# Kernel tuning notes

Hardware: AMD Instinct MI355X
Metric: run time of the kernel (lower is better)

## Reference

```python
import jax, jax.numpy as jnp
import numpy as np
from jax import lax

B, E, K, CAP, NC, TC = 512, 8, 2, 160, 10, 256
EPS = 1e-5
CHANS = [(32, 3), (64, 32), (128, 64), (256, 128)]

def _conv(x, w, b):
    y = lax.conv_general_dilated(x, w, (1, 1), 'SAME', dimension_numbers=('NCHW', 'OIHW', 'NCHW'))
    return y + b[None, :, None, None]

def _bn(x, g, bt, m, v):
    # eval-mode batchnorm with running stats
    s = g / jnp.sqrt(v + EPS)
    return x * s[None, :, None, None] + (bt - m * s)[None, :, None, None]

def _maxpool2(x):
    return lax.reduce_window(x, -jnp.inf, lax.max, (1, 1, 2, 2), (1, 1, 2, 2), 'VALID')

def _trunk(x, ps):
    for i in range(4):
        w, b, g, bt, rm, rv = ps[i]
        x = jax.nn.relu(_bn(_conv(x, w, b), g, bt, rm, rv))
        if i in (1, 3):
            x = _maxpool2(x)
    return x.mean(axis=(2, 3))  # AdaptiveAvgPool2d(1) + Flatten -> [B, TC]

def _route(conf):
    total_needed = B * K
    per_cycle = (total_needed + 3) // 4

    def item_body(c, idx):
        D, ec, sc, assigned, cyc = c
        b, j = idx // E, idx % E
        ok = (~D[b, j]) & (ec[j] < CAP) & (sc[b] < K) & (cyc < per_cycle) & (assigned < total_needed)
        oki = ok.astype(jnp.int32)
        return (D.at[b, j].set(D[b, j] | ok), ec.at[j].add(oki), sc.at[b].add(oki), assigned + oki, cyc + oki), None

    def cycle_body(carry, _):
        D, ec, sc, assigned, current = carry
        order = jnp.argsort(-current.reshape(-1)).astype(jnp.int32)  # descending sort of B*E scores
        (D, ec, sc, assigned, _), _ = lax.scan(item_body, (D, ec, sc, assigned, jnp.int32(0)), order)
        current = conf * (1.0 - ec.astype(jnp.float32) / CAP)[None, :]
        return (D, ec, sc, assigned, current), None

    init = (jnp.zeros((B, E), bool), jnp.zeros((E,), jnp.int32), jnp.zeros((B,), jnp.int32), jnp.int32(0), conf)
    (D, ec, sc, assigned, cur), _ = lax.scan(cycle_body, init, None, length=4)
    return D

def _forward(x, params, cls_w, cls_b):
    feats = _trunk(x, params)                                     # [B, TC]
    logits = jnp.einsum('bd,ecd->bec', feats, cls_w) + cls_b[None]  # [B, E, NC]
    logp = jax.nn.log_softmax(logits, axis=2)
    conf = (jnp.exp(logp) * logp).sum(axis=2)                     # -entropy  [B, E]
    D = _route(lax.stop_gradient(conf))                           # [B, E] bool
    w = jnp.where(D, conf, 0.0)
    final = jnp.einsum('be,bec->bc', w, logits)
    norm = jnp.maximum(D.sum(axis=1, keepdims=True).astype(jnp.float32), 1.0)
    return final / norm, conf, D

def setup_inputs():
    key = jax.random.key(0)
    ks = jax.random.split(key, 8)
    inp = {'x': jax.random.normal(ks[0], (B, 3, 32, 32), jnp.float32)}
    for i, (co, ci) in enumerate(CHANS):
        inp[f'w{i}'] = jax.random.normal(ks[1 + i], (co, ci, 3, 3), jnp.float32) * (2.0 / (ci * 9)) ** 0.5
        inp[f'b{i}'] = jnp.zeros((co,), jnp.float32)
        inp[f'g{i}'] = jnp.ones((co,), jnp.float32)
        inp[f'bt{i}'] = jnp.zeros((co,), jnp.float32)
        inp[f'rm{i}'] = jnp.zeros((co,), jnp.float32)
        inp[f'rv{i}'] = jnp.ones((co,), jnp.float32)
    inp['cls_w'] = jax.random.normal(ks[5], (E, NC, TC), jnp.float32) / TC ** 0.5
    inp['cls_b'] = jnp.zeros((E, NC), jnp.float32)
    return inp

def reference(x, w0, b0, g0, bt0, rm0, rv0, w1, b1, g1, bt1, rm1, rv1, w2, b2, g2, bt2, rm2, rv2, w3, b3, g3, bt3, rm3, rv3, cls_w, cls_b):
    params = [(w0, b0, g0, bt0, rm0, rv0), (w1, b1, g1, bt1, rm1, rv1), (w2, b2, g2, bt2, rm2, rv2), (w3, b3, g3, bt3, rm3, rv3)]
    return _forward(x, params, cls_w, cls_b)
```

## Files before the change

kernel.cpp:

```cpp
#include <hip/hip_runtime.h>
#include <hip/hip_bf16.h>
#include <cstdint>
#include <cstddef>

#define EPSV 1e-5f
typedef unsigned short u16;
using short8 = __attribute__((ext_vector_type(8))) short;
using f32x4  = __attribute__((ext_vector_type(4))) float;

typedef __attribute__((address_space(1))) void* gp1;
typedef __attribute__((address_space(3))) void* lp3;

__device__ __forceinline__ void gload16(const void* g, void* l) {
    __builtin_amdgcn_global_load_lds((gp1)(void*)g, (lp3)l, 16, 0, 0);
}
__device__ __forceinline__ u16 f2bf(float v) {
    __hip_bfloat16 h = __float2bfloat16(v);
    return *reinterpret_cast<u16*>(&h);
}
__device__ __forceinline__ float bf2f(u16 u) {
    __hip_bfloat16 h; *reinterpret_cast<u16*>(&h) = u;
    return __bfloat162float(h);
}

template<int PH2, int PW2, int C>
__global__ __launch_bounds__(256) void ring_kernel(u16* __restrict__ bh, u16* __restrict__ bl)
{
    constexpr int RN = 2 * PW2 + 2 * (PH2 - 2);
    constexpr int C8 = C / 8;
    int id = blockIdx.x * 256 + (int)threadIdx.x;
    if (id >= 512 * RN * C8) return;
    int c8 = id % C8; int t = id / C8;
    int rp = t % RN;  int im = t / RN;
    int py, px;
    if (rp < PW2)            { py = 0;       px = rp; }
    else if (rp < 2 * PW2)   { py = PH2 - 1; px = rp - PW2; }
    else { int rr = rp - 2 * PW2; py = 1 + (rr >> 1); px = (rr & 1) ? (PW2 - 1) : 0; }
    size_t off = ((size_t)(im * PH2 + py) * PW2 + px) * C + c8 * 8;
    uint4 z = {0u, 0u, 0u, 0u};
    *(uint4*)(bh + off) = z;
    *(uint4*)(bl + off) = z;
}

template<int CIN, int COUT>
__global__ __launch_bounds__(256) void wprep_kernel(
    const float* __restrict__ w, const float* __restrict__ b,
    const float* __restrict__ g, const float* __restrict__ bt,
    const float* __restrict__ rm, const float* __restrict__ rv,
    u16* __restrict__ WH, u16* __restrict__ WL, float* __restrict__ bias)
{
    int id = blockIdx.x * 256 + (int)threadIdx.x;
    if (id >= CIN * COUT) return;
    int co = id / CIN, ci = id % CIN;
    float s = g[co] / sqrtf(rv[co] + EPSV);
    #pragma unroll
    for (int k = 0; k < 9; ++k) {
        float v = w[((size_t)co * CIN + ci) * 9 + k] * s;
        u16 hh = f2bf(v);
        size_t o = ((size_t)k * COUT + co) * CIN + ci;
        WH[o] = hh;
        WL[o] = f2bf(v - bf2f(hh));
    }
    if (ci == 0) bias[co] = (b[co] - rm[co]) * s + bt[co];
}

__global__ __launch_bounds__(256) void conv0_kernel(
    const float* __restrict__ x, const float* __restrict__ w,
    const float* __restrict__ bias, const float* __restrict__ g,
    const float* __restrict__ bt, const float* __restrict__ rm,
    const float* __restrict__ rv, u16* __restrict__ Oh, u16* __restrict__ Ol)
{
    const int blk = blockIdx.x;
    const int img = blk >> 2;
    const int p = ((blk & 3) << 8) | (int)threadIdx.x;
    const int y = p >> 5, xx = p & 31;
    const float* xin = x + (size_t)img * 3 * 1024;
    float xv[3][9];
    #pragma unroll
    for (int ci = 0; ci < 3; ++ci)
      #pragma unroll
      for (int ky = 0; ky < 3; ++ky)
        #pragma unroll
        for (int kx = 0; kx < 3; ++kx) {
            int yy = y + ky - 1, xc = xx + kx - 1;
            bool v = (yy >= 0) && (yy < 32) && (xc >= 0) && (xc < 32);
            xv[ci][ky * 3 + kx] = v ? xin[ci * 1024 + yy * 32 + xc] : 0.0f;
        }
    union { u16 u[32]; uint4 v4[4]; } oh, ol;
    #pragma unroll
    for (int co = 0; co < 32; ++co) {
        float s = g[co] / sqrtf(rv[co] + EPSV);
        float c = (bias[co] - rm[co]) * s + bt[co];
        float acc = 0.f;
        #pragma unroll
        for (int ci = 0; ci < 3; ++ci)
          #pragma unroll
          for (int k = 0; k < 9; ++k)
            acc += w[(co * 3 + ci) * 9 + k] * xv[ci][k];
        float v = acc * s + c;
        v = v > 0.f ? v : 0.f;
        u16 hh = f2bf(v);
        oh.u[co] = hh;
        ol.u[co] = f2bf(v - bf2f(hh));
    }
    size_t po = ((size_t)(img * 34 + y + 1) * 34 + xx + 1) * 32;
    #pragma unroll
    for (int q = 0; q < 4; ++q) {
        ((uint4*)(Oh + po))[q] = oh.v4[q];
        ((uint4*)(Ol + po))[q] = ol.v4[q];
    }
}

template<int CIN, int COUT, int H, int W, int BM, int BN, int MODE>
__global__ __launch_bounds__(256, 2) void convM_kernel(
    const u16* __restrict__ Ah, const u16* __restrict__ Al,
    const u16* __restrict__ Wh, const u16* __restrict__ Wl,
    const float* __restrict__ bias,
    u16* __restrict__ Oh, u16* __restrict__ Ol, float* __restrict__ featsPart)
{
    constexpr int KC = CIN / 32;
    constexpr int ROWS = BM / W;
    constexpr int WM = BM / 64;
    constexpr int PW = W + 2;
    constexpr int AT = (ROWS + 2) * PW;
    constexpr int ACH = AT * 4;
    constexpr int BCH = BN * 4;
    constexpr int LW2 = (W == 32) ? 5 : 4;
    constexpr int MPI = (H * W) / BM;

    __shared__ u16 lA[2][AT * 32];
    __shared__ u16 lB[2][BN * 32];

    const int tid = (int)threadIdx.x;
    const int lane = tid & 63;
    const int wv = tid >> 6;
    const int wm = (WM == 4) ? wv : (wv >> 1);
    const int wn = (WM == 4) ? 0 : (wv & 1);
    const int l15 = lane & 15, quad = lane >> 4;

    const int mblk = (int)blockIdx.x, nblk = (int)blockIdx.y;
    const int img = mblk / MPI;
    const int y0 = (mblk % MPI) * ROWS;
    const size_t imgRow = (size_t)img * (H + 2);

    f32x4 acc[4][4];
    f32x4 zz = {0.f, 0.f, 0.f, 0.f};
    #pragma unroll
    for (int i = 0; i < 4; ++i)
      #pragma unroll
      for (int j = 0; j < 4; ++j) acc[i][j] = zz;

    for (int cb = 0; cb < KC; ++cb) {
        __syncthreads();
        #pragma unroll
        for (int it = 0; it < (ACH + 255) / 256; ++it) {
            int id = it * 256 + tid;
            if (id < ACH) {
                int p = id >> 2, s = id & 3;
                int yy = p / PW, xx = p - yy * PW;
                size_t ge = ((imgRow + y0 + yy) * PW + xx) * CIN + cb * 32 + s * 8;
                u16* ld = (u16*)&lA[0][0] + (size_t)(it * 256 + wv * 64) * 8;
                gload16(Ah + ge, ld);
                gload16(Al + ge, ld + AT * 32);
            }
        }
        for (int sh = 0; sh < 9; ++sh) {
            const int ky = sh / 3, kx = sh - 3 * (sh / 3);
            if (sh) __syncthreads();
            #pragma unroll
            for (int it = 0; it < (BCH + 255) / 256; ++it) {
                int id = it * 256 + tid;
                if (id < BCH) {
                    int n = id >> 2, s = id & 3;
                    size_t ge = ((size_t)sh * COUT + nblk * BN + n) * CIN + cb * 32 + s * 8;
                    u16* ld = (u16*)&lB[0][0] + (size_t)(it * 256 + wv * 64) * 8;
                    gload16(Wh + ge, ld);
                    gload16(Wl + ge, ld + BN * 32);
                }
            }
            __syncthreads();
            short8 bh[4], bl[4];
            #pragma unroll
            for (int nt = 0; nt < 4; ++nt) {
                int nrow = wn * 64 + nt * 16 + l15;
                bh[nt] = *(const short8*)&lB[0][nrow * 32 + quad * 8];
                bl[nt] = *(const short8*)&lB[1][nrow * 32 + quad * 8];
            }
            #pragma unroll
            for (int mt = 0; mt < 4; ++mt) {
                int p = wm * 64 + mt * 16 + l15;
                int yl = p >> LW2, xl = p & (W - 1);
                int aoff = ((yl + ky) * PW + xl + kx) * 32 + quad * 8;
                short8 ah = *(const short8*)&lA[0][aoff];
                short8 al = *(const short8*)&lA[1][aoff];
                #pragma unroll
                for (int nt = 0; nt < 4; ++nt) {
                    acc[mt][nt] = __builtin_amdgcn_mfma_f32_16x16x32_bf16(ah, bh[nt], acc[mt][nt], 0, 0, 0);
                    acc[mt][nt] = __builtin_amdgcn_mfma_f32_16x16x32_bf16(ah, bl[nt], acc[mt][nt], 0, 0, 0);
                    acc[mt][nt] = __builtin_amdgcn_mfma_f32_16x16x32_bf16(al, bh[nt], acc[mt][nt], 0, 0, 0);
                }
            }
        }
    }

    if constexpr (MODE == 0) {
        #pragma unroll
        for (int mt = 0; mt < 4; ++mt) {
            int pbase = wm * 64 + mt * 16 + quad * 4;
            int yy = pbase >> LW2;
            #pragma unroll
            for (int nt = 0; nt < 4; ++nt) {
                int n = nblk * BN + wn * 64 + nt * 16 + l15;
                float bs = bias[n];
                #pragma unroll
                for (int r = 0; r < 4; ++r) {
                    int xx = (pbase & (W - 1)) + r;
                    float v = acc[mt][nt][r] + bs; v = v > 0.f ? v : 0.f;
                    size_t oo = ((size_t)(img * (H + 2) + y0 + yy + 1) * (W + 2) + xx + 1) * COUT + n;
                    u16 hh = f2bf(v);
                    Oh[oo] = hh;
                    Ol[oo] = f2bf(v - bf2f(hh));
                }
            }
        }
    } else if constexpr (MODE == 1) {
        #pragma unroll
        for (int nt = 0; nt < 4; ++nt) {
            int n = nt * 16 + l15;
            float bs = bias[n];
            #pragma unroll
            for (int mb = 0; mb < 2; ++mb) {
                #pragma unroll
                for (int xp = 0; xp < 2; ++xp) {
                    float v = fmaxf(fmaxf(acc[mb][nt][2 * xp], acc[mb][nt][2 * xp + 1]),
                                    fmaxf(acc[mb + 2][nt][2 * xp], acc[mb + 2][nt][2 * xp + 1]));
                    v += bs; v = v > 0.f ? v : 0.f;
                    int py = (y0 >> 1) + wm;
                    int px = mb * 8 + quad * 2 + xp;
                    size_t oo = ((size_t)(img * 18 + py + 1) * 18 + px + 1) * COUT + n;
                    u16 hh = f2bf(v);
                    Oh[oo] = hh;
                    Ol[oo] = f2bf(v - bf2f(hh));
                }
            }
        }
    } else {
        __shared__ float fbuf[2][128];
        #pragma unroll
        for (int nt = 0; nt < 4; ++nt) {
            float bs = bias[nblk * BN + wn * 64 + nt * 16 + l15];
            float s = 0.f;
            #pragma unroll
            for (int mp = 0; mp < 2; ++mp)
              #pragma unroll
              for (int xp = 0; xp < 2; ++xp) {
                  float v = fmaxf(fmaxf(acc[2 * mp][nt][2 * xp], acc[2 * mp][nt][2 * xp + 1]),
                                  fmaxf(acc[2 * mp + 1][nt][2 * xp], acc[2 * mp + 1][nt][2 * xp + 1]));
                  v += bs; v = v > 0.f ? v : 0.f;
                  s += v;
              }
            s += __shfl_xor(s, 16, 64);
            s += __shfl_xor(s, 32, 64);
            if (quad == 0) fbuf[wm][wn * 64 + nt * 16 + l15] = s;
        }
        __syncthreads();
        if (tid < 128) {
            float f = (fbuf[0][tid] + fbuf[1][tid]) * (1.0f / 64.0f);
            featsPart[((size_t)(mblk % MPI) * 512 + img) * 256 + nblk * BN + tid] = f;
        }
    }
}

__global__ __launch_bounds__(128) void head_kernel(
    const float* __restrict__ featsPart, const float* __restrict__ cls_w,
    const float* __restrict__ cls_b, float* __restrict__ logits,
    float* __restrict__ conf)
{
    __shared__ float f[256];
    __shared__ float wt[80 * 65];
    __shared__ float lg[80];
    const int b = blockIdx.x, tid = (int)threadIdx.x;
    f[tid]       = featsPart[b * 256 + tid]       + featsPart[131072 + b * 256 + tid];
    f[tid + 128] = featsPart[b * 256 + tid + 128] + featsPart[131072 + b * 256 + tid + 128];
    float acc = 0.f;
    for (int ch = 0; ch < 4; ++ch) {
        __syncthreads();
        for (int q = tid; q < 80 * 64; q += 128) {
            int r = q >> 6, cc = q & 63;
            wt[r * 65 + cc] = cls_w[r * 256 + ch * 64 + cc];
        }
        __syncthreads();
        if (tid < 80) {
            #pragma unroll 8
            for (int dd = 0; dd < 64; ++dd)
                acc += wt[tid * 65 + dd] * f[ch * 64 + dd];
        }
    }
    if (tid < 80) {
        acc += cls_b[tid];
        logits[b * 80 + tid] = acc;
        lg[tid] = acc;
    }
    __syncthreads();
    if (tid < 80 && (tid % 10) == 0) {
        const int e = tid / 10;
        float m = lg[e * 10];
        for (int cc = 1; cc < 10; ++cc) m = fmaxf(m, lg[e * 10 + cc]);
        float ssum = 0.f;
        for (int cc = 0; cc < 10; ++cc) ssum += expf(lg[e * 10 + cc] - m);
        float lz = m + logf(ssum);
        float cf = 0.f;
        for (int cc = 0; cc < 10; ++cc) {
            float lp = lg[e * 10 + cc] - lz;
            cf += expf(lp) * lp;
        }
        conf[b * 8 + e] = cf;
    }
}

__global__ __launch_bounds__(1024) void route_kernel(
    const float* __restrict__ confG,
    const float* __restrict__ logitsG,
    float* __restrict__ outv)
{
    __shared__ float val[4096];
    __shared__ unsigned short sidx[4096];
    __shared__ unsigned char Dls[512];
    __shared__ int ec[8];
    __shared__ int assignedS;
    const int tid = (int)threadIdx.x;
    if (tid < 512) Dls[tid] = 0;
    if (tid < 8) ec[tid] = 0;
    if (tid == 0) assignedS = 0;
    __syncthreads();

    for (int cycle = 0; cycle < 4; ++cycle) {
        for (int t = tid; t < 4096; t += 1024) {
            float sc = 1.0f - ((float)ec[t & 7]) / 160.0f;
            val[t] = confG[t] * sc;
            sidx[t] = (unsigned short)t;
        }
        for (int k = 2; k <= 4096; k <<= 1)
            for (int j = k >> 1; j > 0; j >>= 1) {
                __syncthreads();
                for (int t = tid; t < 2048; t += 1024) {
                    int i = ((t & ~(j - 1)) << 1) | (t & (j - 1));
                    int p = i | j;
                    float va = val[i], vb = val[p];
                    unsigned short ia = sidx[i], ib = sidx[p];
                    bool first = (va > vb) || (va == vb && ia < ib);
                    bool up = (i & k) == 0;
                    if (up ? !first : first) {
                        val[i] = vb; val[p] = va; sidx[i] = ib; sidx[p] = ia;
                    }
                }
            }
        __syncthreads();
        if (tid < 64) {
            const int lane = tid;
            int cyc = 0;
            int assigned = assignedS;
            for (int chunk = 0; chunk < 64; ++chunk) {
                if (cyc >= 256 || assigned >= 1024) break;
                int i = (chunk << 6) | lane;
                int id = sidx[i];
                int b = id >> 3, j = id & 7;
                unsigned d = Dls[b];
                bool notA = ((d >> j) & 1) == 0;
                int ecj = ec[j];
                int scb = __popc(d & 255);
                unsigned long long sb = ~0ull;
                #pragma unroll
                for (int t2 = 0; t2 < 9; ++t2) {
                    unsigned long long bl = __ballot((b >> t2) & 1);
                    sb &= ((b >> t2) & 1) ? bl : ~bl;
                }
                unsigned long long jb0 = __ballot(j & 1);
                unsigned long long jb1 = __ballot((j >> 1) & 1);
                unsigned long long jb2 = __ballot((j >> 2) & 1);
                unsigned long long sj = ((j & 1) ? jb0 : ~jb0) &
                                        ((j & 2) ? jb1 : ~jb1) &
                                        ((j & 4) ? jb2 : ~jb2);
                unsigned long long earlier = (1ull << lane) - 1ull;
                bool ok = notA && (ecj < 160) && (scb < 2);
                unsigned long long okm = __ballot(ok);
                for (int it = 0; it < 64; ++it) {
                    unsigned long long em = okm & earlier;
                    int aE = __popcll(em & sj);
                    int aS = __popcll(em & sb);
                    int aC = __popcll(em);
                    bool ok2 = notA && (ecj + aE) < 160 && (scb + aS) < 2 &&
                               (cyc + aC) < 256 && (assigned + aC) < 1024;
                    unsigned long long okm2 = __ballot(ok2);
                    ok = ok2;
                    if (okm2 == okm) break;
                    okm = okm2;
                }
                int add = __popcll(okm);
                if (lane < 8) {
                    unsigned long long mj = ((lane & 1) ? jb0 : ~jb0) &
                                            ((lane & 2) ? jb1 : ~jb1) &
                                            ((lane & 4) ? jb2 : ~jb2);
                    int c2 = __popcll(mj & okm);
                    if (c2) ec[lane] += c2;
                }
                if (ok) {
                    unsigned long long grp = okm & sb;
                    if (lane == __builtin_ctzll(grp)) {
                        unsigned orb = 0;
                        #pragma unroll
                        for (int jj = 0; jj < 8; ++jj) {
                            unsigned long long mj2 = ((jj & 1) ? jb0 : ~jb0) &
                                                     ((jj & 2) ? jb1 : ~jb1) &
                                                     ((jj & 4) ? jb2 : ~jb2);
                            if (mj2 & grp) orb |= (1u << jj);
                        }
                        Dls[b] = (unsigned char)(d | orb);
                    }
                }
                cyc += add;
                assigned += add;
                __threadfence_block();
            }
            if (lane == 0) assignedS = assigned;
        }
        __syncthreads();
    }

    for (int o = tid; o < 5120; o += 1024) {
        int b = o / 10, c = o - b * 10;
        unsigned d = Dls[b];
        float norm = fmaxf((float)__popc(d & 255), 1.0f);
        float sum = 0.f;
        #pragma unroll
        for (int e = 0; e < 8; ++e)
            if ((d >> e) & 1)
                sum += confG[b * 8 + e] * logitsG[(b * 8 + e) * 10 + c];
        outv[o] = sum / norm;
    }
    for (int t = tid; t < 4096; t += 1024) {
        outv[5120 + t] = confG[t];
        outv[9216 + t] = (float)((Dls[t >> 3] >> (t & 7)) & 1);
    }
}

extern "C" void kernel_launch(void* const* d_in, const int* in_sizes, int n_in,
                              void* d_out, int out_size, void* d_ws, size_t ws_size,
                              hipStream_t stream)
{
    const float* x    = (const float*)d_in[0];
    const float* w0   = (const float*)d_in[1];
    const float* b0   = (const float*)d_in[2];
    const float* g0   = (const float*)d_in[3];
    const float* bt0  = (const float*)d_in[4];
    const float* rm0  = (const float*)d_in[5];
    const float* rv0  = (const float*)d_in[6];
    const float* w1   = (const float*)d_in[7];
    const float* b1   = (const float*)d_in[8];
    const float* g1   = (const float*)d_in[9];
    const float* bt1  = (const float*)d_in[10];
    const float* rm1  = (const float*)d_in[11];
    const float* rv1  = (const float*)d_in[12];
    const float* w2   = (const float*)d_in[13];
    const float* b2   = (const float*)d_in[14];
    const float* g2   = (const float*)d_in[15];
    const float* bt2  = (const float*)d_in[16];
    const float* rm2  = (const float*)d_in[17];
    const float* rv2  = (const float*)d_in[18];
    const float* w3   = (const float*)d_in[19];
    const float* b3   = (const float*)d_in[20];
    const float* g3   = (const float*)d_in[21];
    const float* bt3  = (const float*)d_in[22];
    const float* rm3  = (const float*)d_in[23];
    const float* rv3  = (const float*)d_in[24];
    const float* cls_w = (const float*)d_in[25];
    const float* cls_b = (const float*)d_in[26];
    float* outp = (float*)d_out;

    char* ws = (char*)d_ws;
    u16* A1H = (u16*)(ws);
    u16* A1L = (u16*)(ws + 21233664);
    u16* A0H = (u16*)(ws + 42467328);
    u16* A0L = (u16*)(ws + 42467328 + 37879808);
    u16* A2H = (u16*)(ws + 42467328);
    u16* A2L = (u16*)(ws + 42467328 + 42467328);
    u16* W1H = (u16*)(ws + 127401984);
    u16* W1L = (u16*)(ws + 127438848);
    u16* W2H = (u16*)(ws + 127475712);
    u16* W2L = (u16*)(ws + 127623168);
    u16* W3H = (u16*)(ws + 127770624);
    u16* W3L = (u16*)(ws + 128360448);
    float* BS1 = (float*)(ws + 128950272);
    float* BS2 = (float*)(ws + 128950528);
    float* BS3 = (float*)(ws + 128951040);
    float* featsPart = (float*)(ws + 128952064);
    float* logits    = (float*)(ws + 130000640);
    float* conf      = (float*)(ws + 130164480);

    ring_kernel<34, 34, 32><<<(512 * 132 * 4 + 255) / 256, 256, 0, stream>>>(A0H, A0L);
    ring_kernel<18, 18, 64><<<(512 * 68 * 8 + 255) / 256, 256, 0, stream>>>(A1H, A1L);
    wprep_kernel<32, 64><<<8, 256, 0, stream>>>(w1, b1, g1, bt1, rm1, rv1, W1H, W1L, BS1);
    wprep_kernel<64, 128><<<32, 256, 0, stream>>>(w2, b2, g2, bt2, rm2, rv2, W2H, W2L, BS2);
    wprep_kernel<128, 256><<<128, 256, 0, stream>>>(w3, b3, g3, bt3, rm3, rv3, W3H, W3L, BS3);

    conv0_kernel<<<2048, 256, 0, stream>>>(x, w0, b0, g0, bt0, rm0, rv0, A0H, A0L);
    convM_kernel<32, 64, 32, 32, 256, 64, 1>
        <<<dim3(2048, 1), 256, 0, stream>>>(A0H, A0L, W1H, W1L, BS1, A1H, A1L, nullptr);
    ring_kernel<18, 18, 128><<<(512 * 68 * 16 + 255) / 256, 256, 0, stream>>>(A2H, A2L);
    convM_kernel<64, 128, 16, 16, 128, 128, 0>
        <<<dim3(1024, 1), 256, 0, stream>>>(A1H, A1L, W2H, W2L, BS2, A2H, A2L, nullptr);
    convM_kernel<128, 256, 16, 16, 128, 128, 2>
        <<<dim3(1024, 2), 256, 0, stream>>>(A2H, A2L, W3H, W3L, BS3, nullptr, nullptr, featsPart);
    head_kernel<<<512, 128, 0, stream>>>(featsPart, cls_w, cls_b, logits, conf);
    route_kernel<<<1, 1024, 0, stream>>>(conf, logits, outp);
}
```

Baseline: 726.6 us.

## Presort per-expert confidences once and merge sorted lists each routing cycle

Adds a presort kernel that bitonic-sorts each expert's 512 confidences once. Since the per-cycle capacity scaling is a positive factor per expert, each column's order is unchanged across cycles. Each routing cycle then rescales the values and does three merge-path passes to combine the 8 sorted lists, instead of a full 4096-element bitonic sort. This cuts the barrier-heavy single-block sort cost but adds a kernel launch and more shared memory.

```diff
diff --git a/kernel.cpp b/kernel.cpp
--- a/kernel.cpp
+++ b/kernel.cpp
@@ -318,43 +318,98 @@
     }
 }
 
+__global__ __launch_bounds__(256) void presort_kernel(
+    const float* __restrict__ confG, u16* __restrict__ sidx0)
+{
+    __shared__ float v[512];
+    __shared__ u16 bi[512];
+    const int j = (int)blockIdx.x, tid = (int)threadIdx.x;
+    for (int r = tid; r < 512; r += 256) { v[r] = confG[r * 8 + j]; bi[r] = (u16)r; }
+    for (int k = 2; k <= 512; k <<= 1)
+        for (int jj = k >> 1; jj > 0; jj >>= 1) {
+            __syncthreads();
+            int i = ((tid & ~(jj - 1)) << 1) | (tid & (jj - 1));
+            int p = i | jj;
+            float va = v[i], vb = v[p];
+            u16 ia = bi[i], ib = bi[p];
+            bool first = (va > vb) || (va == vb && ia < ib);
+            bool up = (i & k) == 0;
+            if (up ? !first : first) { v[i] = vb; v[p] = va; bi[i] = ib; bi[p] = ia; }
+        }
+    __syncthreads();
+    for (int r = tid; r < 512; r += 256)
+        sidx0[j * 512 + r] = (u16)(bi[r] * 8 + j);
+}
+
 __global__ __launch_bounds__(1024) void route_kernel(
     const float* __restrict__ confG,
     const float* __restrict__ logitsG,
+    const u16*   __restrict__ sidx0,
     float* __restrict__ outv)
 {
-    __shared__ float val[4096];
-    __shared__ unsigned short sidx[4096];
+    __shared__ float valById[4096];
+    __shared__ float sv[4096];
+    __shared__ u16 P[4096];
+    __shared__ u16 mA[4096];
+    __shared__ u16 mB[4096];
     __shared__ unsigned char Dls[512];
     __shared__ int ec[8];
     __shared__ int assignedS;
     const int tid = (int)threadIdx.x;
+
+    for (int t = tid; t < 4096; t += 1024) {
+        valById[t] = confG[t];
+        P[t] = sidx0[t];
+    }
     if (tid < 512) Dls[tid] = 0;
     if (tid < 8) ec[tid] = 0;
     if (tid == 0) assignedS = 0;
-    __syncthreads();
+
+    auto earlier = [&](u16 a, u16 b) -> bool {
+        float va = sv[a], vb = sv[b];
+        return (va > vb) || (va == vb && a < b);
+    };
+    auto mergeChunk = [&](const u16* X, const u16* Y, int n, int o0, u16* out) {
+        int lo = o0 - n; if (lo < 0) lo = 0;
+        int hi = o0 < n ? o0 : n;
+        while (lo < hi) {
+            int mid = (lo + hi) >> 1;
+            if (earlier(X[mid], Y[o0 - 1 - mid])) lo = mid + 1; else hi = mid;
+        }
+        int i = lo, jj = o0 - lo;
+        #pragma unroll
+        for (int q = 0; q < 4; ++q) {
+            u16 xc = X[i < n ? i : (n - 1)];
+            u16 yc = Y[jj < n ? jj : (n - 1)];
+            bool takeX = (jj >= n) || ((i < n) && earlier(xc, yc));
+            out[q] = takeX ? xc : yc;
+            if (takeX) ++i; else ++jj;
+        }
+    };
 
     for (int cycle = 0; cycle < 4; ++cycle) {
+        __syncthreads();
         for (int t = tid; t < 4096; t += 1024) {
             float sc = 1.0f - ((float)ec[t & 7]) / 160.0f;
-            val[t] = confG[t] * sc;
-            sidx[t] = (unsigned short)t;
-        }
-        for (int k = 2; k <= 4096; k <<= 1)
-            for (int j = k >> 1; j > 0; j >>= 1) {
-                __syncthreads();
-                for (int t = tid; t < 2048; t += 1024) {
-                    int i = ((t & ~(j - 1)) << 1) | (t & (j - 1));
-                    int p = i | j;
-                    float va = val[i], vb = val[p];
-                    unsigned short ia = sidx[i], ib = sidx[p];
-                    bool first = (va > vb) || (va == vb && ia < ib);
-                    bool up = (i & k) == 0;
-                    if (up ? !first : first) {
-                        val[i] = vb; val[p] = va; sidx[i] = ib; sidx[p] = ia;
-                    }
-                }
-            }
+            sv[t] = valById[t] * sc;
+        }
+        __syncthreads();
+        {
+            int g = tid << 2;
+            int p = g >> 10, o0 = g & 1023;
+            mergeChunk(&P[(p << 1) * 512], &P[(p << 1) * 512 + 512], 512, o0, &mA[(p << 10) + o0]);
+        }
+        __syncthreads();
+        {
+            int g = tid << 2;
+            int p = g >> 11, o0 = g & 2047;
+            mergeChunk(&mA[p << 11], &mA[(p << 11) + 1024], 1024, o0, &mB[(p << 11) + o0]);
+        }
+        __syncthreads();
+        {
+            int o0 = tid << 2;
+            mergeChunk(&mB[0], &mB[2048], 2048, o0, &mA[o0]);
+        }
         __syncthreads();
         if (tid < 64) {
             const int lane = tid;
@@ -362,8 +417,7 @@
             int assigned = assignedS;
             for (int chunk = 0; chunk < 64; ++chunk) {
                 if (cyc >= 256 || assigned >= 1024) break;
-                int i = (chunk << 6) | lane;
-                int id = sidx[i];
+                int id = mA[(chunk << 6) | lane];
                 int b = id >> 3, j = id & 7;
                 unsigned d = Dls[b];
                 bool notA = ((d >> j) & 1) == 0;
@@ -381,11 +435,11 @@
                 unsigned long long sj = ((j & 1) ? jb0 : ~jb0) &
                                         ((j & 2) ? jb1 : ~jb1) &
                                         ((j & 4) ? jb2 : ~jb2);
-                unsigned long long earlier = (1ull << lane) - 1ull;
+                unsigned long long earlierM = (1ull << lane) - 1ull;
                 bool ok = notA && (ecj < 160) && (scb < 2);
                 unsigned long long okm = __ballot(ok);
                 for (int it = 0; it < 64; ++it) {
-                    unsigned long long em = okm & earlier;
+                    unsigned long long em = okm & earlierM;
                     int aE = __popcll(em & sj);
                     int aS = __popcll(em & sb);
                     int aC = __popcll(em);
@@ -409,11 +463,11 @@
                     if (lane == __builtin_ctzll(grp)) {
                         unsigned orb = 0;
                         #pragma unroll
-                        for (int jj = 0; jj < 8; ++jj) {
-                            unsigned long long mj2 = ((jj & 1) ? jb0 : ~jb0) &
-                                                     ((jj & 2) ? jb1 : ~jb1) &
-                                                     ((jj & 4) ? jb2 : ~jb2);
-                            if (mj2 & grp) orb |= (1u << jj);
+                        for (int jj2 = 0; jj2 < 8; ++jj2) {
+                            unsigned long long mj2 = ((jj2 & 1) ? jb0 : ~jb0) &
+                                                     ((jj2 & 2) ? jb1 : ~jb1) &
+                                                     ((jj2 & 4) ? jb2 : ~jb2);
+                            if (mj2 & grp) orb |= (1u << jj2);
                         }
                         Dls[b] = (unsigned char)(d | orb);
                     }
@@ -424,8 +478,8 @@
             }
             if (lane == 0) assignedS = assigned;
         }
-        __syncthreads();
-    }
+    }
+    __syncthreads();
 
     for (int o = tid; o < 5120; o += 1024) {
         int b = o / 10, c = o - b * 10;
@@ -496,6 +550,7 @@
     float* featsPart = (float*)(ws + 128952064);
     float* logits    = (float*)(ws + 130000640);
     float* conf      = (float*)(ws + 130164480);
+    u16* sidx0 = (u16*)(ws + 42467328);
 
     ring_kernel<34, 34, 32><<<(512 * 132 * 4 + 255) / 256, 256, 0, stream>>>(A0H, A0L);
     ring_kernel<18, 18, 64><<<(512 * 68 * 8 + 255) / 256, 256, 0, stream>>>(A1H, A1L);
@@ -512,5 +567,6 @@
     convM_kernel<128, 256, 16, 16, 128, 128, 2>
         <<<dim3(1024, 2), 256, 0, stream>>>(A2H, A2L, W3H, W3L, BS3, nullptr, nullptr, featsPart);
     head_kernel<<<512, 128, 0, stream>>>(featsPart, cls_w, cls_b, logits, conf);
-    route_kernel<<<1, 1024, 0, stream>>>(conf, logits, outp);
-}
+    presort_kernel<<<8, 256, 0, stream>>>(conf, sidx0);
+    route_kernel<<<1, 1024, 0, stream>>>(conf, logits, sidx0, outp);
+}
```

New measurement: 613.1 us. -15.6%, faster.
